# Kernel optimization log

Hardware: AMD Instinct MI355X
Metric: run time of the kernel (lower is better)

## Reference

```python
import math
import jax, jax.numpy as jnp
import numpy as np

B, D, N, K = 16, 512, 2048, 32  # batch, latent_dim, n points, k feature width


def setup_inputs() -> dict:
    key = jax.random.key(0)
    ks = jax.random.split(key, 11)
    s = 0.02
    return {
        "x": jax.random.normal(ks[0], (B, D), jnp.float32),
        "WQ": jax.random.normal(ks[1], (D, N * K), jnp.float32) * s,
        "bQ": jax.random.normal(ks[2], (N * K,), jnp.float32) * s,
        "WK": jax.random.normal(ks[3], (D, N * K), jnp.float32) * s,
        "bK": jax.random.normal(ks[4], (N * K,), jnp.float32) * s,
        "WV": jax.random.normal(ks[5], (D, N * K), jnp.float32) * s,
        "bV": jax.random.normal(ks[6], (N * K,), jnp.float32) * s,
        "Wout": jax.random.normal(ks[7], (3, K), jnp.float32) * s,
        "bout": jax.random.normal(ks[8], (3,), jnp.float32) * s,
        "Wori": jax.random.normal(ks[9], (3, K), jnp.float32) * s,
        "bori": jax.random.normal(ks[10], (3,), jnp.float32) * s,
    }


def reference(x, WQ, bQ, WK, bK, WV, bV, Wout, bout, Wori, bori):
    b = x.shape[0]
    q = (x @ WQ + bQ).reshape(b, N, K)   # fc_Q output, used for both Q and ori
    k = (x @ WK + bK).reshape(b, N, K)
    v = (x @ WV + bV).reshape(b, N, K)
    # conv_ori is a pointwise Conv1d(K, 3, 1) applied to ori^T -> [b,3,N];
    # computed in [b,N,3] layout (final output layout after the last transpose).
    ori = jnp.einsum('bnk,ck->bnc', q, Wori) + bori  # [b, N, 3]
    # single-head scaled dot-product attention, scores [b, N, N]
    scores = jnp.einsum('bnk,bmk->bnm', q, k) / math.sqrt(K)
    attn = jax.nn.softmax(scores, axis=2)
    out = jnp.einsum('bnm,bmk->bnk', attn, v)        # [b, N, K]
    out = jnp.einsum('bnk,ck->bnc', out, Wout) + bout  # pointwise conv_output
    return out + ori                                 # [b, N, 3]
```

## Files before the change

### kernel.cpp

```cpp
#include <hip/hip_runtime.h>
#include <hip/hip_bf16.h>
#include <math.h>

#define NB 16
#define ND 512
#define NN 2048
#define NKF 32
#define NNK 65536

typedef short s8v __attribute__((ext_vector_type(8)));
typedef float f4v __attribute__((ext_vector_type(4)));
typedef unsigned short u16;
typedef unsigned int u32;
typedef u16 u16x8 __attribute__((ext_vector_type(8)));
typedef u32 u32x4 __attribute__((ext_vector_type(4)));

__device__ __forceinline__ u16 f2bf(float x) {
    u32 u = __builtin_bit_cast(u32, x);
    return (u16)((u + 0x7fffu + ((u >> 16) & 1u)) >> 16);
}
__device__ __forceinline__ float bf2f(u16 b) {
    u32 u = ((u32)b) << 16;
    return __builtin_bit_cast(float, u);
}

__global__ __launch_bounds__(256) void proj_partial(
    const float* __restrict__ x,
    const float* __restrict__ WQ, const float* __restrict__ WK,
    const float* __restrict__ WV, u16* __restrict__ part)
{
    const int t = threadIdx.x;
    const int jb = blockIdx.x;
    const int mat = blockIdx.y;
    const int dz = blockIdx.z;
    const float* __restrict__ W = (mat == 0) ? WQ : (mat == 1) ? WK : WV;
    const int j = jb * 1024 + t * 4;
    const int d0 = dz * 128;

    float4 acc[16];
    #pragma unroll
    for (int b = 0; b < 16; b++) acc[b] = make_float4(0.f, 0.f, 0.f, 0.f);

    const float* wp = W + (size_t)d0 * NNK + j;
    const float* xp = x + d0;

    float4 wa[8], wb[8];
    #pragma unroll
    for (int u = 0; u < 8; u++) wa[u] = *(const float4*)(wp + (size_t)u * NNK);

    #pragma unroll 1
    for (int dd = 0; dd < 128; dd += 16) {
        #pragma unroll
        for (int u = 0; u < 8; u++)
            wb[u] = *(const float4*)(wp + (size_t)(dd + 8 + u) * NNK);
        __builtin_amdgcn_sched_barrier(0);

        #pragma unroll
        for (int u = 0; u < 8; u++) {
            const float* xr = xp + dd + u;
            #pragma unroll
            for (int b = 0; b < 16; b++) {
                float xv = xr[b * ND];
                acc[b].x = fmaf(xv, wa[u].x, acc[b].x);
                acc[b].y = fmaf(xv, wa[u].y, acc[b].y);
                acc[b].z = fmaf(xv, wa[u].z, acc[b].z);
                acc[b].w = fmaf(xv, wa[u].w, acc[b].w);
            }
        }

        if (dd + 16 < 128) {
            #pragma unroll
            for (int u = 0; u < 8; u++)
                wa[u] = *(const float4*)(wp + (size_t)(dd + 16 + u) * NNK);
        }
        __builtin_amdgcn_sched_barrier(0);

        #pragma unroll
        for (int u = 0; u < 8; u++) {
            const float* xr = xp + dd + 8 + u;
            #pragma unroll
            for (int b = 0; b < 16; b++) {
                float xv = xr[b * ND];
                acc[b].x = fmaf(xv, wb[u].x, acc[b].x);
                acc[b].y = fmaf(xv, wb[u].y, acc[b].y);
                acc[b].z = fmaf(xv, wb[u].z, acc[b].z);
                acc[b].w = fmaf(xv, wb[u].w, acc[b].w);
            }
        }
    }

    size_t base = ((size_t)(mat * 4 + dz) * 16) * NNK + j;
    #pragma unroll
    for (int b = 0; b < 16; b++) {
        u32 lo = (u32)f2bf(acc[b].x) | ((u32)f2bf(acc[b].y) << 16);
        u32 hi = (u32)f2bf(acc[b].z) | ((u32)f2bf(acc[b].w) << 16);
        *(uint2*)(part + base + (size_t)b * NNK) = make_uint2(lo, hi);
    }
}

__global__ __launch_bounds__(256) void reduce_cast(
    const u16* __restrict__ part,
    const float* __restrict__ bQ, const float* __restrict__ bK,
    const float* __restrict__ bV,
    u16* __restrict__ qb, u16* __restrict__ kb, u16* __restrict__ vT)
{
    const int t = threadIdx.x;
    const int jc = blockIdx.x;
    const int b  = blockIdx.y;
    const int mat = blockIdx.z;
    const float* __restrict__ bias = (mat == 0) ? bQ : (mat == 1) ? bK : bV;
    const int j = jc * 2048 + t * 8;

    float4 b0 = *(const float4*)(bias + j);
    float4 b1 = *(const float4*)(bias + j + 4);
    float v[8] = {b0.x, b0.y, b0.z, b0.w, b1.x, b1.y, b1.z, b1.w};

    #pragma unroll
    for (int dz = 0; dz < 4; dz++) {
        size_t p = ((size_t)(mat * 4 + dz) * 16 + b) * NNK + j;
        u16x8 pp = *(const u16x8*)(part + p);
        #pragma unroll
        for (int i = 0; i < 8; i++) v[i] += bf2f(pp[i]);
    }

    const float scale = (mat == 1) ? 0.2550868230023389f : 1.0f;
    u16 h[8];
    #pragma unroll
    for (int i = 0; i < 8; i++) h[i] = f2bf(v[i] * scale);

    __shared__ u16 vt[32][72];

    if (mat < 2) {
        u16* dst = ((mat == 0) ? qb : kb) + (size_t)b * NNK + j;
        u16x8 hv;
        #pragma unroll
        for (int i = 0; i < 8; i++) hv[i] = h[i];
        *(u16x8*)dst = hv;
    } else {
        const int n  = t >> 2;
        const int k0 = (t & 3) * 8;
        #pragma unroll
        for (int i = 0; i < 8; i++) vt[k0 + i][n] = h[i];
        __syncthreads();
        const int k  = t >> 3;
        const int c8 = t & 7;
        u16x8 ov;
        #pragma unroll
        for (int i = 0; i < 8; i++) ov[i] = vt[k][c8 * 8 + i];
        u16* dst = vT + (size_t)b * NNK + (size_t)k * NN + jc * 64 + c8 * 8;
        *(u16x8*)dst = ov;
    }
}

__global__ __launch_bounds__(256) void attn_kernel(
    const u16* __restrict__ qb, const u16* __restrict__ kb,
    const u16* __restrict__ vT,
    const float* __restrict__ Wout, const float* __restrict__ bout,
    const float* __restrict__ Wori, const float* __restrict__ bori,
    float* __restrict__ out)
{
    const int t = threadIdx.x;
    const int w = t >> 6;
    const int l = t & 63;
    const int g = l >> 4;
    const int n = l & 15;
    const int b = blockIdx.y;
    const int q0 = blockIdx.x * 64;

    __shared__ __align__(16) u16 Ks[2][2048];
    __shared__ __align__(16) u16 Vs[2][2048];

    const u16* qrow = qb + (size_t)b * NNK + (size_t)(q0 + w * 16 + n) * NKF + g * 8;
    const s8v qf = *(const s8v*)qrow;

    const int krow = t >> 2, kcol = (t & 3) * 8;
    const int vrow = t >> 3, vslot = t & 7;
    const int vcolL = (vslot ^ (vrow & 7)) * 8;
    const u16* kgp = kb + (size_t)b * NNK + (size_t)krow * NKF + kcol;
    const u16* vgp = vT + (size_t)b * NNK + (size_t)vrow * NN + vcolL;

    s8v kreg, vreg;
    kreg = *(const s8v*)(kgp);                 vreg = *(const s8v*)(vgp);
    *(s8v*)(&Ks[0][t * 8]) = kreg;             *(s8v*)(&Vs[0][t * 8]) = vreg;
    kreg = *(const s8v*)(kgp + (size_t)2048);  vreg = *(const s8v*)(vgp + 64);
    __syncthreads();

    float m_run = -INFINITY, l_run = 0.f;
    f4v O0 = {0.f, 0.f, 0.f, 0.f}, O1 = {0.f, 0.f, 0.f, 0.f};
    const bool hi = (l >= 32);
    const int srcA = ((2 * g) & 3) * 16 + n;
    const int srcB = ((2 * g + 1) & 3) * 16 + n;

    for (int it = 0; it < 32; it++) {
        const int cur = it & 1;
        if (it + 1 < 32) {
            *(s8v*)(&Ks[cur ^ 1][t * 8]) = kreg;
            *(s8v*)(&Vs[cur ^ 1][t * 8]) = vreg;
        }
        if (it + 2 < 32) {
            kreg = *(const s8v*)(kgp + (size_t)(it + 2) * 2048);
            vreg = *(const s8v*)(vgp + (size_t)(it + 2) * 64);
        }

        f4v S[4];
        #pragma unroll
        for (int tt = 0; tt < 4; tt++) {
            s8v ka = *(const s8v*)(&Ks[cur][(n + 16 * tt) * NKF + g * 8]);
            f4v z = {0.f, 0.f, 0.f, 0.f};
            S[tt] = __builtin_amdgcn_mfma_f32_16x16x32_bf16(ka, qf, z, 0, 0, 0);
        }

        float pmax = -INFINITY;
        #pragma unroll
        for (int tt = 0; tt < 4; tt++)
            #pragma unroll
            for (int r = 0; r < 4; r++) pmax = fmaxf(pmax, S[tt][r]);
        pmax = fmaxf(pmax, __shfl_xor(pmax, 16));
        pmax = fmaxf(pmax, __shfl_xor(pmax, 32));
        const float m_new = fmaxf(m_run, pmax);
        const float corr = exp2f(m_run - m_new);

        float p[4][4];
        float tsum = 0.f;
        #pragma unroll
        for (int tt = 0; tt < 4; tt++)
            #pragma unroll
            for (int r = 0; r < 4; r++) {
                p[tt][r] = exp2f(S[tt][r] - m_new);
                tsum += p[tt][r];
            }
        tsum += __shfl_xor(tsum, 16);
        tsum += __shfl_xor(tsum, 32);
        l_run = l_run * corr + tsum;
        m_run = m_new;
        #pragma unroll
        for (int r = 0; r < 4; r++) { O0[r] *= corr; O1[r] *= corr; }

        u32 pk[4][2];
        #pragma unroll
        for (int tt = 0; tt < 4; tt++) {
            pk[tt][0] = (u32)f2bf(p[tt][0]) | ((u32)f2bf(p[tt][1]) << 16);
            pk[tt][1] = (u32)f2bf(p[tt][2]) | ((u32)f2bf(p[tt][3]) << 16);
        }

        #pragma unroll
        for (int kc = 0; kc < 2; kc++) {
            u32 lo0 = (u32)__shfl((int)pk[2 * kc][0], srcA);
            u32 hi0 = (u32)__shfl((int)pk[2 * kc + 1][0], srcA);
            u32 lo1 = (u32)__shfl((int)pk[2 * kc][1], srcA);
            u32 hi1 = (u32)__shfl((int)pk[2 * kc + 1][1], srcA);
            u32 lo2 = (u32)__shfl((int)pk[2 * kc][0], srcB);
            u32 hi2 = (u32)__shfl((int)pk[2 * kc + 1][0], srcB);
            u32 lo3 = (u32)__shfl((int)pk[2 * kc][1], srcB);
            u32 hi3 = (u32)__shfl((int)pk[2 * kc + 1][1], srcB);
            u32x4 fr;
            fr.x = hi ? hi0 : lo0;
            fr.y = hi ? hi1 : lo1;
            fr.z = hi ? hi2 : lo2;
            fr.w = hi ? hi3 : lo3;
            s8v pa = __builtin_bit_cast(s8v, fr);

            {
                int row = n;
                int slot = (g + 4 * kc) ^ (row & 7);
                s8v va = *(const s8v*)(&Vs[cur][row * 64 + slot * 8]);
                O0 = __builtin_amdgcn_mfma_f32_16x16x32_bf16(va, pa, O0, 0, 0, 0);
            }
            {
                int row = n + 16;
                int slot = (g + 4 * kc) ^ (row & 7);
                s8v va = *(const s8v*)(&Vs[cur][row * 64 + slot * 8]);
                O1 = __builtin_amdgcn_mfma_f32_16x16x32_bf16(va, pa, O1, 0, 0, 0);
            }
        }
        __syncthreads();
    }

    const float inv = 1.0f / l_run;
    float po[3] = {0.f, 0.f, 0.f};
    #pragma unroll
    for (int r = 0; r < 4; r++) {
        int dk0 = 4 * g + r;
        int dk1 = 16 + 4 * g + r;
        float o0 = O0[r] * inv;
        float o1 = O1[r] * inv;
        #pragma unroll
        for (int c = 0; c < 3; c++) {
            po[c] += o0 * Wout[c * NKF + dk0];
            po[c] += o1 * Wout[c * NKF + dk1];
        }
    }
    #pragma unroll
    for (int e = 0; e < 8; e++) {
        float qv = bf2f((u16)qf[e]);
        int k = 8 * g + e;
        #pragma unroll
        for (int c = 0; c < 3; c++) po[c] += qv * Wori[c * NKF + k];
    }
    #pragma unroll
    for (int c = 0; c < 3; c++) {
        po[c] += __shfl_xor(po[c], 16);
        po[c] += __shfl_xor(po[c], 32);
    }
    if (g == 0) {
        int row = q0 + w * 16 + n;
        size_t o = ((size_t)b * NN + row) * 3;
        #pragma unroll
        for (int c = 0; c < 3; c++) out[o + c] = po[c] + bout[c] + bori[c];
    }
}

extern "C" void kernel_launch(void* const* d_in, const int* in_sizes, int n_in,
                              void* d_out, int out_size, void* d_ws, size_t ws_size,
                              hipStream_t stream) {
    const float* x    = (const float*)d_in[0];
    const float* WQ   = (const float*)d_in[1];
    const float* bQ   = (const float*)d_in[2];
    const float* WK   = (const float*)d_in[3];
    const float* bK   = (const float*)d_in[4];
    const float* WV   = (const float*)d_in[5];
    const float* bV   = (const float*)d_in[6];
    const float* Wout = (const float*)d_in[7];
    const float* bout = (const float*)d_in[8];
    const float* Wori = (const float*)d_in[9];
    const float* bori = (const float*)d_in[10];
    float* out = (float*)d_out;

    char* ws = (char*)d_ws;
    u16* part = (u16*)ws;
    u16* qb = (u16*)(ws + 25165824);
    u16* kb = (u16*)(ws + 25165824 + 2097152);
    u16* vT = (u16*)(ws + 25165824 + 2 * 2097152);

    proj_partial<<<dim3(64, 3, 4), 256, 0, stream>>>(x, WQ, WK, WV, part);
    reduce_cast<<<dim3(32, 16, 3), 256, 0, stream>>>(part, bQ, bK, bV, qb, kb, vT);
    attn_kernel<<<dim3(32, 16), 256, 0, stream>>>(qb, kb, vT, Wout, bout, Wori, bori, out);
}
```

Measured before the change: 132.1 us.

## Stream projection weights via async global-to-LDS double buffering and stage x in LDS

The projection kernel now loads weight rows straight into a double-buffered LDS stage with global_load_lds, instead of prefetching them into registers. x is staged once per block into LDS in transposed form and read as float4 vectors, replacing scalar global loads. The goal is to overlap weight streaming with the FMA work and cut register pressure and global load instructions. In exchange it adds per-chunk block barriers and hand-written waitcnt logic, which must match the number of outstanding loads exactly.

```diff
diff --git a/kernel.cpp b/kernel.cpp
--- a/kernel.cpp
+++ b/kernel.cpp
@@ -24,72 +24,93 @@
     return __builtin_bit_cast(float, u);
 }
 
+__device__ __forceinline__ void gload_lds16(const void* g, void* l) {
+    __builtin_amdgcn_global_load_lds(
+        (const __attribute__((address_space(1))) void*)g,
+        (__attribute__((address_space(3))) void*)l, 16, 0, 0);
+}
+
 __global__ __launch_bounds__(256) void proj_partial(
     const float* __restrict__ x,
     const float* __restrict__ WQ, const float* __restrict__ WK,
     const float* __restrict__ WV, u16* __restrict__ part)
 {
     const int t = threadIdx.x;
+    const int w = t >> 6;
+    const int lane = t & 63;
     const int jb = blockIdx.x;
     const int mat = blockIdx.y;
     const int dz = blockIdx.z;
     const float* __restrict__ W = (mat == 0) ? WQ : (mat == 1) ? WK : WV;
-    const int j = jb * 1024 + t * 4;
+    const int j0 = jb * 1024;
     const int d0 = dz * 128;
 
+    __shared__ __align__(16) float Wstage[2][8][1024];
+    __shared__ __align__(16) float xs[128][16];
+
+    for (int i = t; i < 2048; i += 256) {
+        int b = i & 15, d = i >> 4;
+        xs[d][b] = x[b * ND + d0 + d];
+    }
+
     float4 acc[16];
     #pragma unroll
     for (int b = 0; b < 16; b++) acc[b] = make_float4(0.f, 0.f, 0.f, 0.f);
 
-    const float* wp = W + (size_t)d0 * NNK + j;
-    const float* xp = x + d0;
-
-    float4 wa[8], wb[8];
-    #pragma unroll
-    for (int u = 0; u < 8; u++) wa[u] = *(const float4*)(wp + (size_t)u * NNK);
+    const int NCHUNK = 16;
+    auto stage = [&](int c, int buf) {
+        const float* cbase = W + (size_t)(d0 + c * 8) * NNK + j0;
+        #pragma unroll
+        for (int s = 0; s < 8; s++) {
+            int r = w * 2 + (s >> 2);
+            int colq = (s & 3) * 256;
+            const float* src = cbase + (size_t)r * NNK + colq + lane * 4;
+            void* dst = (void*)&Wstage[buf][r][colq];
+            gload_lds16(src, dst);
+        }
+    };
+
+    stage(0, 0);
+    stage(1, 1);
 
     #pragma unroll 1
-    for (int dd = 0; dd < 128; dd += 16) {
-        #pragma unroll
-        for (int u = 0; u < 8; u++)
-            wb[u] = *(const float4*)(wp + (size_t)(dd + 8 + u) * NNK);
+    for (int c = 0; c < NCHUNK; c++) {
+        const int buf = c & 1;
+        if (c + 1 < NCHUNK) {
+            asm volatile("s_waitcnt vmcnt(8) lgkmcnt(0)" ::: "memory");
+        } else {
+            asm volatile("s_waitcnt vmcnt(0) lgkmcnt(0)" ::: "memory");
+        }
         __builtin_amdgcn_sched_barrier(0);
-
-        #pragma unroll
-        for (int u = 0; u < 8; u++) {
-            const float* xr = xp + dd + u;
+        __builtin_amdgcn_s_barrier();
+        __builtin_amdgcn_sched_barrier(0);
+
+        #pragma unroll
+        for (int r = 0; r < 8; r++) {
+            const int dd = c * 8 + r;
+            float xv[16];
+            #pragma unroll
+            for (int q = 0; q < 4; q++)
+                *(float4*)&xv[q * 4] = *(const float4*)&xs[dd][q * 4];
+            float4 wv = *(const float4*)&Wstage[buf][r][t * 4];
             #pragma unroll
             for (int b = 0; b < 16; b++) {
-                float xv = xr[b * ND];
-                acc[b].x = fmaf(xv, wa[u].x, acc[b].x);
-                acc[b].y = fmaf(xv, wa[u].y, acc[b].y);
-                acc[b].z = fmaf(xv, wa[u].z, acc[b].z);
-                acc[b].w = fmaf(xv, wa[u].w, acc[b].w);
+                acc[b].x = fmaf(xv[b], wv.x, acc[b].x);
+                acc[b].y = fmaf(xv[b], wv.y, acc[b].y);
+                acc[b].z = fmaf(xv[b], wv.z, acc[b].z);
+                acc[b].w = fmaf(xv[b], wv.w, acc[b].w);
             }
         }
 
-        if (dd + 16 < 128) {
-            #pragma unroll
-            for (int u = 0; u < 8; u++)
-                wa[u] = *(const float4*)(wp + (size_t)(dd + 16 + u) * NNK);
-        }
+        asm volatile("s_waitcnt lgkmcnt(0)" ::: "memory");
         __builtin_amdgcn_sched_barrier(0);
-
-        #pragma unroll
-        for (int u = 0; u < 8; u++) {
-            const float* xr = xp + dd + 8 + u;
-            #pragma unroll
-            for (int b = 0; b < 16; b++) {
-                float xv = xr[b * ND];
-                acc[b].x = fmaf(xv, wb[u].x, acc[b].x);
-                acc[b].y = fmaf(xv, wb[u].y, acc[b].y);
-                acc[b].z = fmaf(xv, wb[u].z, acc[b].z);
-                acc[b].w = fmaf(xv, wb[u].w, acc[b].w);
-            }
-        }
-    }
-
-    size_t base = ((size_t)(mat * 4 + dz) * 16) * NNK + j;
+        __builtin_amdgcn_s_barrier();
+        __builtin_amdgcn_sched_barrier(0);
+
+        if (c + 2 < NCHUNK) stage(c + 2, buf);
+    }
+
+    size_t base = ((size_t)(mat * 4 + dz) * 16) * NNK + j0 + t * 4;
     #pragma unroll
     for (int b = 0; b < 16; b++) {
         u32 lo = (u32)f2bf(acc[b].x) | ((u32)f2bf(acc[b].y) << 16);
```

Result: slower. 150.3 us (+13.8%).
